# Kernel tuning notes

Hardware: AMD Instinct MI355X
Metric: run time of the kernel (lower is better)

The kernel has to match this reference:

```python
import jax, jax.numpy as jnp
import numpy as np

TOP_K = 4

def _silu_and_mul(gu):
    g, u = jnp.split(gu, 2, axis=-1)
    return jax.nn.silu(g) * u

def setup_inputs() -> dict:
    key = jax.random.key(0)
    ks = jax.random.split(key, 7)
    H, E, I, Is = 2048, 16, 1408, 5632
    s = 0.02
    return {
        "hidden_states": jax.random.normal(ks[0], (4, 1024, H), dtype=jnp.float32),
        "gate_w": jax.random.normal(ks[1], (E, H), dtype=jnp.float32) * s,
        "sgate_w": jax.random.normal(ks[2], (1, H), dtype=jnp.float32) * s,
        "w13": jax.random.normal(ks[3], (E, 2 * I, H), dtype=jnp.float32) * s,
        "w2": jax.random.normal(ks[4], (E, H, I), dtype=jnp.float32) * s,
        "shared_gate_up_w": jax.random.normal(ks[5], (2 * Is, H), dtype=jnp.float32) * s,
        "shared_down_w": jax.random.normal(ks[6], (H, Is), dtype=jnp.float32) * s,
    }

def reference(hidden_states, gate_w, sgate_w, w13, w2, shared_gate_up_w, shared_down_w):
    B, S, H = hidden_states.shape
    x = hidden_states.reshape(-1, H)  # [M, H]
    E = gate_w.shape[0]

    # shared expert: SiluAndMul MLP gated by sigmoid(shared_expert_gate(x))
    shared = _silu_and_mul(x @ shared_gate_up_w.T) @ shared_down_w.T
    shared = shared * jax.nn.sigmoid(x @ sgate_w.T)  # [M, H]

    # router: softmax in fp32, top-k (NOT renormalized, per original code)
    router_logits = x @ gate_w.T
    routing_weights = jax.nn.softmax(router_logits.astype(jnp.float32), axis=-1)
    topk_w, topk_ids = jax.lax.top_k(routing_weights, TOP_K)  # [M, K]

    # loop over fixed expert set via scan; every token goes through each
    # expert, masked by its routing coefficient (0 if not routed)
    def body(acc, ew):
        w13_e, w2_e, e = ew
        coef = jnp.sum(jnp.where(topk_ids == e, topk_w, 0.0), axis=-1)  # [M]
        h = _silu_and_mul(x @ w13_e.T)  # [M, I]
        acc = acc + (h @ w2_e.T).astype(jnp.float32) * coef[:, None]
        return acc, None

    init = jnp.zeros((x.shape[0], H), dtype=jnp.float32)
    sparse_out, _ = jax.lax.scan(body, init, (w13, w2, jnp.arange(E)))
    out = shared + sparse_out.astype(x.dtype)
    return out.reshape(B, S, H)
```

## Files before the change

kernel.cpp:

```cpp
#include <hip/hip_runtime.h>
#include <hip/hip_bf16.h>

#define E_NUM 16
#define TOPK 4
#define H_DIM 2048
#define I_DIM 1408
#define IS_DIM 5632
#define M_TOK 4096

typedef __attribute__((ext_vector_type(8))) short short8;
typedef __attribute__((ext_vector_type(4))) float f32x4;

static __device__ __forceinline__ unsigned short f2bf(float f) {
    unsigned int u = __float_as_uint(f);
    unsigned int r = (u + 0x7FFFu + ((u >> 16) & 1u)) >> 16;
    return (unsigned short)r;
}

static __device__ __forceinline__ void gl16(const unsigned short* g, unsigned short* l) {
    __builtin_amdgcn_global_load_lds(
        (const __attribute__((address_space(1))) unsigned int*)g,
        (__attribute__((address_space(3))) unsigned int*)l, 16, 0, 0);
}

__global__ __launch_bounds__(256) void k_router(
    const float* __restrict__ x, const float* __restrict__ gw,
    const float* __restrict__ sgw, int* __restrict__ counts,
    int* __restrict__ ltok, float* __restrict__ lcoef, float* __restrict__ sg)
{
    const int wid = threadIdx.x >> 6, lane = threadIdx.x & 63;
    const int t = blockIdx.x * 4 + wid;
    const float* xr = x + (size_t)t * H_DIM;
    float xv[32];
#pragma unroll
    for (int i = 0; i < 32; ++i) xv[i] = xr[i * 64 + lane];

    float lg[E_NUM];
    for (int e = 0; e < E_NUM; ++e) {
        const float* g = gw + (size_t)e * H_DIM;
        float s = 0.f;
#pragma unroll
        for (int i = 0; i < 32; ++i) s += xv[i] * g[i * 64 + lane];
#pragma unroll
        for (int off = 32; off; off >>= 1) s += __shfl_xor(s, off);
        lg[e] = s;
    }
    {
        float s = 0.f;
#pragma unroll
        for (int i = 0; i < 32; ++i) s += xv[i] * sgw[i * 64 + lane];
#pragma unroll
        for (int off = 32; off; off >>= 1) s += __shfl_xor(s, off);
        if (lane == 0) sg[t] = 1.f / (1.f + __expf(-s));
    }
    float mx = lg[0];
#pragma unroll
    for (int e = 1; e < E_NUM; ++e) mx = fmaxf(mx, lg[e]);
    float sum = 0.f, w[E_NUM];
#pragma unroll
    for (int e = 0; e < E_NUM; ++e) { w[e] = __expf(lg[e] - mx); sum += w[e]; }
    float inv = 1.f / sum;
#pragma unroll
    for (int e = 0; e < E_NUM; ++e) w[e] *= inv;

    if (lane == 0) {
        for (int j = 0; j < TOPK; ++j) {
            float best = -1.f; int bi = 0;
            for (int e = 0; e < E_NUM; ++e) if (w[e] > best) { best = w[e]; bi = e; }
            int pos = atomicAdd(&counts[bi], 1);
            ltok[bi * M_TOK + pos]  = t;
            lcoef[bi * M_TOK + pos] = best;
            w[bi] = -2.f;
        }
    }
}

__global__ void k_prefix(const int* __restrict__ counts, int* __restrict__ base) {
    if (threadIdx.x == 0) {
        int a = 0;
        for (int e = 0; e < E_NUM; ++e) { base[e] = a; a += counts[e]; }
        base[E_NUM] = a;
    }
}

__global__ __launch_bounds__(256) void k_cvtw(const float* __restrict__ src,
                                              unsigned short* __restrict__ dst, size_t n8)
{
    size_t stride = (size_t)gridDim.x * 256;
    for (size_t t = (size_t)blockIdx.x * 256 + threadIdx.x; t < n8; t += stride) {
        size_t i = t * 8;
        float4 a = *(const float4*)(src + i);
        float4 b = *(const float4*)(src + i + 4);
        union { unsigned short u[8]; short8 v; } o;
        o.u[0] = f2bf(a.x); o.u[1] = f2bf(a.y); o.u[2] = f2bf(a.z); o.u[3] = f2bf(a.w);
        o.u[4] = f2bf(b.x); o.u[5] = f2bf(b.y); o.u[6] = f2bf(b.z); o.u[7] = f2bf(b.w);
        *(short8*)(dst + i) = o.v;
    }
}

template<int MODE, int BN, int KDIM, int NOFF, long long BSTR, int KSPLIT>
__global__ __launch_bounds__(512, 2) void k_gemm(
    const unsigned short* __restrict__ Abase,
    const unsigned short* __restrict__ Bbase,
    void* __restrict__ outp,
    const int* __restrict__ ltok, const float* __restrict__ lcoef,
    const int* __restrict__ counts, const int* __restrict__ basearr,
    const float* __restrict__ sg)
{
    constexpr bool DUAL = (MODE == 0 || MODE == 2);
    constexpr int NFR = BN / 64;
    constexpr int KCH = KDIM / KSPLIT;

    extern __shared__ unsigned short smem[];
    unsigned short* sA = smem;
    unsigned short* sB = smem + 32768;

    const int tid = threadIdx.x;
    const int lane = tid & 63, wid = tid >> 6;
    const int wr = wid >> 2, wcol = wid & 3;
    const int lr = lane & 15, lk = lane >> 4;

    const unsigned gx = gridDim.x, gy = gridDim.y;
    const unsigned nwg = gx * gy;
    const unsigned orig = blockIdx.y * gx + blockIdx.x;
    const unsigned q8 = nwg >> 3, r8 = nwg & 7;
    const unsigned xcd = orig & 7, off8 = orig >> 3;
    const unsigned wg = ((xcd < r8) ? xcd * (q8 + 1) : r8 * (q8 + 1) + (xcd - r8) * q8) + off8;
    const int n0 = (int)(wg / gy) * BN;
    const int r0 = (int)(wg % gy) * 256;
    const int e  = blockIdx.z;

    int cnt = M_TOK, gbase = 0;
    if constexpr (MODE == 2 || MODE == 3) {
        cnt = counts[e];
        if (r0 >= cnt) return;
        gbase = basearr[e];
    }
    const int kbeg = (KSPLIT > 1) ? e * KCH : 0;
    const unsigned short* Bexp = Bbase + (size_t)e * (size_t)BSTR;

    const unsigned short* aptr[4];
    const unsigned short* bptr[4];
#pragma unroll
    for (int i = 0; i < 4; ++i) {
        const int c = i * 512 + tid;
        const int row = c >> 3, c8 = c & 7;
        int ar;
        if constexpr (MODE == 0 || MODE == 1) ar = r0 + row;
        else {
            int rr = r0 + row; if (rr > cnt - 1) rr = cnt - 1;
            ar = (MODE == 2) ? ltok[e * M_TOK + rr] : (gbase + rr);
        }
        aptr[i] = Abase + (size_t)ar * KDIM + kbeg + ((c8 ^ (row & 7)) << 3);
        int br;
        if constexpr (DUAL) br = (row < 128) ? (n0 + row) : (NOFF + n0 + row - 128);
        else br = n0 + row;
        bptr[i] = Bexp + (size_t)br * KDIM + kbeg + ((c8 ^ (row & 7)) << 3);
    }

    f32x4 acc[8][NFR];
    f32x4 accu[DUAL ? 8 : 1][NFR];
    const f32x4 z = {0.f, 0.f, 0.f, 0.f};
#pragma unroll
    for (int m = 0; m < 8; ++m)
#pragma unroll
        for (int n = 0; n < NFR; ++n) { acc[m][n] = z; if constexpr (DUAL) accu[m][n] = z; }

    auto STAGE = [&](int buf, int kt) {
        const int bo = buf << 14;
#pragma unroll
        for (int i = 0; i < 4; ++i) gl16(aptr[i] + kt, &sA[bo + ((i * 512 + tid) << 3)]);
#pragma unroll
        for (int i = 0; i < 4; ++i) gl16(bptr[i] + kt, &sB[bo + ((i * 512 + tid) << 3)]);
    };

    STAGE(0, 0);
    __syncthreads();
    int cur = 0;
#pragma unroll 1
    for (int kt = 0; kt < KCH; kt += 64) {
        if (kt + 64 < KCH) STAGE(cur ^ 1, kt + 64);
        __builtin_amdgcn_s_setprio(1);
#pragma unroll
        for (int kk = 0; kk < 2; ++kk) {
            const int c8 = kk * 4 + lk;
            short8 af[8];
#pragma unroll
            for (int m = 0; m < 8; ++m) {
                const int row = wr * 128 + m * 16 + lr;
                af[m] = *(const short8*)&sA[(cur << 14) + (row << 6) + ((c8 ^ (row & 7)) << 3)];
            }
#pragma unroll
            for (int n = 0; n < NFR; ++n) {
                const int rowb = wcol * (BN / 4) + n * 16 + lr;
                short8 bf = *(const short8*)&sB[(cur << 14) + (rowb << 6) + ((c8 ^ (rowb & 7)) << 3)];
#pragma unroll
                for (int m = 0; m < 8; ++m)
                    acc[m][n] = __builtin_amdgcn_mfma_f32_16x16x32_bf16(af[m], bf, acc[m][n], 0, 0, 0);
                if constexpr (DUAL) {
                    const int rowu = rowb + 128;
                    short8 bu = *(const short8*)&sB[(cur << 14) + (rowu << 6) + ((c8 ^ (rowu & 7)) << 3)];
#pragma unroll
                    for (int m = 0; m < 8; ++m)
                        accu[m][n] = __builtin_amdgcn_mfma_f32_16x16x32_bf16(af[m], bu, accu[m][n], 0, 0, 0);
                }
            }
        }
        __builtin_amdgcn_s_setprio(0);
        __syncthreads();
        cur ^= 1;
    }

    const int colbase = n0 + wcol * (BN / 4);
#pragma unroll
    for (int m = 0; m < 8; ++m) {
#pragma unroll
        for (int j = 0; j < 4; ++j) {
            const int r = wr * 128 + m * 16 + lk * 4 + j;
            if constexpr (MODE == 0) {
                size_t orow = (size_t)(r0 + r) * IS_DIM;
#pragma unroll
                for (int n = 0; n < NFR; ++n) {
                    int col = colbase + n * 16 + lr;
                    float g = acc[m][n][j];
                    float h = g / (1.f + __expf(-g)) * accu[m][n][j];
                    ((unsigned short*)outp)[orow + col] = f2bf(h);
                }
            } else if constexpr (MODE == 2) {
                if (r0 + r < cnt) {
                    size_t orow = (size_t)(gbase + r0 + r) * I_DIM;
#pragma unroll
                    for (int n = 0; n < NFR; ++n) {
                        int col = colbase + n * 16 + lr;
                        float g = acc[m][n][j];
                        float h = g / (1.f + __expf(-g)) * accu[m][n][j];
                        ((unsigned short*)outp)[orow + col] = f2bf(h);
                    }
                }
            } else if constexpr (MODE == 1) {
                int tok = r0 + r;
                float scale = sg[tok];
                size_t orow = (size_t)tok * H_DIM;
#pragma unroll
                for (int n = 0; n < NFR; ++n) {
                    int col = colbase + n * 16 + lr;
                    atomicAdd((float*)outp + orow + col, acc[m][n][j] * scale);
                }
            } else {
                if (r0 + r < cnt) {
                    int tok = ltok[e * M_TOK + r0 + r];
                    float scale = lcoef[e * M_TOK + r0 + r];
                    size_t orow = (size_t)tok * H_DIM;
#pragma unroll
                    for (int n = 0; n < NFR; ++n) {
                        int col = colbase + n * 16 + lr;
                        atomicAdd((float*)outp + orow + col, acc[m][n][j] * scale);
                    }
                }
            }
        }
    }
}

extern "C" void kernel_launch(void* const* d_in, const int* in_sizes, int n_in,
                              void* d_out, int out_size, void* d_ws, size_t ws_size,
                              hipStream_t stream) {
    const float* x    = (const float*)d_in[0];
    const float* gw   = (const float*)d_in[1];
    const float* sgw  = (const float*)d_in[2];
    const float* w13  = (const float*)d_in[3];
    const float* w2   = (const float*)d_in[4];
    const float* sguw = (const float*)d_in[5];
    const float* sdw  = (const float*)d_in[6];
    float* out = (float*)d_out;

    char* ws = (char*)d_ws;
    unsigned short* xb    = (unsigned short*)ws;
    unsigned short* hbuf  = (unsigned short*)(ws + 16777216);
    unsigned short* w13b  = (unsigned short*)(ws + 62914560);
    unsigned short* w2b   = (unsigned short*)(ws + 247463936);
    unsigned short* sguwb = (unsigned short*)(ws + 339738624);
    unsigned short* sdwb  = (unsigned short*)(ws + 385875968);
    size_t so = 408944640ULL;
    int*   ltok   = (int*)  (ws + so);
    float* lcoef  = (float*)(ws + so + 262144);
    int*   counts = (int*)  (ws + so + 524288);
    int*   basep  = (int*)  (ws + so + 524288 + 256);
    float* sg     = (float*)(ws + so + 524288 + 512);

    hipMemsetAsync(counts, 0, 64, stream);
    hipMemsetAsync(out, 0, (size_t)out_size * sizeof(float), stream);
    k_router<<<M_TOK / 4, 256, 0, stream>>>(x, gw, sgw, counts, ltok, lcoef, sg);
    k_prefix<<<1, 64, 0, stream>>>(counts, basep);
    k_cvtw<<<4096, 256, 0, stream>>>(x, xb, (size_t)M_TOK * H_DIM / 8);
    k_cvtw<<<8192, 256, 0, stream>>>(sguw, sguwb, (size_t)2 * IS_DIM * H_DIM / 8);
    k_cvtw<<<8192, 256, 0, stream>>>(sdw,  sdwb,  (size_t)H_DIM * IS_DIM / 8);
    k_cvtw<<<8192, 256, 0, stream>>>(w13,  w13b,  (size_t)E_NUM * 2 * I_DIM * H_DIM / 8);
    k_cvtw<<<8192, 256, 0, stream>>>(w2,   w2b,   (size_t)E_NUM * H_DIM * I_DIM / 8);

    static const int DYN = 131072;
    (void)hipFuncSetAttribute(reinterpret_cast<const void*>(&k_gemm<0, 128, 2048, IS_DIM, 0LL, 1>),
                              hipFuncAttributeMaxDynamicSharedMemorySize, DYN);
    (void)hipFuncSetAttribute(reinterpret_cast<const void*>(&k_gemm<1, 256, 5632, 0, 0LL, 2>),
                              hipFuncAttributeMaxDynamicSharedMemorySize, DYN);
    (void)hipFuncSetAttribute(reinterpret_cast<const void*>(&k_gemm<2, 128, 2048, I_DIM, 5767168LL, 1>),
                              hipFuncAttributeMaxDynamicSharedMemorySize, DYN);
    (void)hipFuncSetAttribute(reinterpret_cast<const void*>(&k_gemm<3, 256, 1408, 0, 2883584LL, 1>),
                              hipFuncAttributeMaxDynamicSharedMemorySize, DYN);

    k_gemm<0, 128, 2048, IS_DIM, 0LL, 1>
        <<<dim3(IS_DIM / 128, M_TOK / 256, 1), 512, DYN, stream>>>(
            xb, sguwb, hbuf, ltok, lcoef, counts, basep, sg);
    k_gemm<1, 256, 5632, 0, 0LL, 2>
        <<<dim3(H_DIM / 256, M_TOK / 256, 2), 512, DYN, stream>>>(
            hbuf, sdwb, out, ltok, lcoef, counts, basep, sg);
    k_gemm<2, 128, 2048, I_DIM, 5767168LL, 1>
        <<<dim3(I_DIM / 128, M_TOK / 256, E_NUM), 512, DYN, stream>>>(
            xb, w13b, hbuf, ltok, lcoef, counts, basep, sg);
    k_gemm<3, 256, 1408, 0, 2883584LL, 1>
        <<<dim3(H_DIM / 256, M_TOK / 256, E_NUM), 512, DYN, stream>>>(
            hbuf, w2b, out, ltok, lcoef, counts, basep, sg);
}
```

Baseline: 1.215 ms.

## Shrink GEMM tiles to 128x128 with 256 threads and single-buffered static LDS

Reworks the grouped GEMM kernel from 256-row tiles with 512 threads and double-buffered dynamic shared memory to 128x128 tiles with 256 threads and a single static LDS buffer. The intent is more workgroups and higher occupancy, which also wastes fewer padded rows for the variable per-expert token counts. In exchange it drops the prefetch overlap, so each K step now waits on its global loads before computing. Smaller tiles also mean less operand reuse per LDS load and more atomic traffic in the down projections.

```diff
diff --git a/kernel.cpp b/kernel.cpp
--- a/kernel.cpp
+++ b/kernel.cpp
@@ -98,8 +98,8 @@
     }
 }
 
-template<int MODE, int BN, int KDIM, int NOFF, long long BSTR, int KSPLIT>
-__global__ __launch_bounds__(512, 2) void k_gemm(
+template<int MODE, int KDIM, int NOFF, long long BSTR, int KSPLIT>
+__global__ __launch_bounds__(256, 2) void k_gemm(
     const unsigned short* __restrict__ Abase,
     const unsigned short* __restrict__ Bbase,
     void* __restrict__ outp,
@@ -108,16 +108,13 @@
     const float* __restrict__ sg)
 {
     constexpr bool DUAL = (MODE == 0 || MODE == 2);
-    constexpr int NFR = BN / 64;
+    constexpr int BROWS = DUAL ? 256 : 128;
+    constexpr int NB = BROWS / 32;
     constexpr int KCH = KDIM / KSPLIT;
-
-    extern __shared__ unsigned short smem[];
-    unsigned short* sA = smem;
-    unsigned short* sB = smem + 32768;
 
     const int tid = threadIdx.x;
     const int lane = tid & 63, wid = tid >> 6;
-    const int wr = wid >> 2, wcol = wid & 3;
+    const int wr = wid >> 1, wc = wid & 1;
     const int lr = lane & 15, lk = lane >> 4;
 
     const unsigned gx = gridDim.x, gy = gridDim.y;
@@ -126,8 +123,8 @@
     const unsigned q8 = nwg >> 3, r8 = nwg & 7;
     const unsigned xcd = orig & 7, off8 = orig >> 3;
     const unsigned wg = ((xcd < r8) ? xcd * (q8 + 1) : r8 * (q8 + 1) + (xcd - r8) * q8) + off8;
-    const int n0 = (int)(wg / gy) * BN;
-    const int r0 = (int)(wg % gy) * 256;
+    const int n0 = (int)(wg / gy) * 128;
+    const int r0 = (int)(wg % gy) * 128;
     const int e  = blockIdx.z;
 
     int cnt = M_TOK, gbase = 0;
@@ -139,11 +136,13 @@
     const int kbeg = (KSPLIT > 1) ? e * KCH : 0;
     const unsigned short* Bexp = Bbase + (size_t)e * (size_t)BSTR;
 
+    __shared__ unsigned short sA[128 * 64];
+    __shared__ unsigned short sB[BROWS * 64];
+
     const unsigned short* aptr[4];
-    const unsigned short* bptr[4];
 #pragma unroll
     for (int i = 0; i < 4; ++i) {
-        const int c = i * 512 + tid;
+        const int c = i * 256 + tid;
         const int row = c >> 3, c8 = c & 7;
         int ar;
         if constexpr (MODE == 0 || MODE == 1) ar = r0 + row;
@@ -152,75 +151,73 @@
             ar = (MODE == 2) ? ltok[e * M_TOK + rr] : (gbase + rr);
         }
         aptr[i] = Abase + (size_t)ar * KDIM + kbeg + ((c8 ^ (row & 7)) << 3);
+    }
+    const unsigned short* bptr[NB];
+#pragma unroll
+    for (int i = 0; i < NB; ++i) {
+        const int c = i * 256 + tid;
+        const int row = c >> 3, c8 = c & 7;
         int br;
         if constexpr (DUAL) br = (row < 128) ? (n0 + row) : (NOFF + n0 + row - 128);
         else br = n0 + row;
         bptr[i] = Bexp + (size_t)br * KDIM + kbeg + ((c8 ^ (row & 7)) << 3);
     }
 
-    f32x4 acc[8][NFR];
-    f32x4 accu[DUAL ? 8 : 1][NFR];
+    f32x4 acc[4][4];
+    f32x4 accu[DUAL ? 4 : 1][4];
     const f32x4 z = {0.f, 0.f, 0.f, 0.f};
 #pragma unroll
-    for (int m = 0; m < 8; ++m)
-#pragma unroll
-        for (int n = 0; n < NFR; ++n) { acc[m][n] = z; if constexpr (DUAL) accu[m][n] = z; }
-
-    auto STAGE = [&](int buf, int kt) {
-        const int bo = buf << 14;
-#pragma unroll
-        for (int i = 0; i < 4; ++i) gl16(aptr[i] + kt, &sA[bo + ((i * 512 + tid) << 3)]);
-#pragma unroll
-        for (int i = 0; i < 4; ++i) gl16(bptr[i] + kt, &sB[bo + ((i * 512 + tid) << 3)]);
-    };
-
-    STAGE(0, 0);
-    __syncthreads();
-    int cur = 0;
+    for (int m = 0; m < 4; ++m)
+#pragma unroll
+        for (int n = 0; n < 4; ++n) { acc[m][n] = z; if constexpr (DUAL) accu[m][n] = z; }
+
 #pragma unroll 1
     for (int kt = 0; kt < KCH; kt += 64) {
-        if (kt + 64 < KCH) STAGE(cur ^ 1, kt + 64);
+#pragma unroll
+        for (int i = 0; i < 4; ++i) gl16(aptr[i] + kt, &sA[(i * 256 + tid) << 3]);
+#pragma unroll
+        for (int i = 0; i < NB; ++i) gl16(bptr[i] + kt, &sB[(i * 256 + tid) << 3]);
+        __syncthreads();
         __builtin_amdgcn_s_setprio(1);
 #pragma unroll
         for (int kk = 0; kk < 2; ++kk) {
             const int c8 = kk * 4 + lk;
-            short8 af[8];
-#pragma unroll
-            for (int m = 0; m < 8; ++m) {
-                const int row = wr * 128 + m * 16 + lr;
-                af[m] = *(const short8*)&sA[(cur << 14) + (row << 6) + ((c8 ^ (row & 7)) << 3)];
+            short8 af[4];
+#pragma unroll
+            for (int m = 0; m < 4; ++m) {
+                const int row = wr * 64 + m * 16 + lr;
+                af[m] = *(const short8*)&sA[(row << 6) + ((c8 ^ (row & 7)) << 3)];
             }
 #pragma unroll
-            for (int n = 0; n < NFR; ++n) {
-                const int rowb = wcol * (BN / 4) + n * 16 + lr;
-                short8 bf = *(const short8*)&sB[(cur << 14) + (rowb << 6) + ((c8 ^ (rowb & 7)) << 3)];
-#pragma unroll
-                for (int m = 0; m < 8; ++m)
+            for (int n = 0; n < 4; ++n) {
+                const int rowb = wc * 64 + n * 16 + lr;
+                short8 bf = *(const short8*)&sB[(rowb << 6) + ((c8 ^ (rowb & 7)) << 3)];
+#pragma unroll
+                for (int m = 0; m < 4; ++m)
                     acc[m][n] = __builtin_amdgcn_mfma_f32_16x16x32_bf16(af[m], bf, acc[m][n], 0, 0, 0);
                 if constexpr (DUAL) {
                     const int rowu = rowb + 128;
-                    short8 bu = *(const short8*)&sB[(cur << 14) + (rowu << 6) + ((c8 ^ (rowu & 7)) << 3)];
-#pragma unroll
-                    for (int m = 0; m < 8; ++m)
+                    short8 bu = *(const short8*)&sB[(rowu << 6) + ((c8 ^ (rowu & 7)) << 3)];
+#pragma unroll
+                    for (int m = 0; m < 4; ++m)
                         accu[m][n] = __builtin_amdgcn_mfma_f32_16x16x32_bf16(af[m], bu, accu[m][n], 0, 0, 0);
                 }
             }
         }
         __builtin_amdgcn_s_setprio(0);
         __syncthreads();
-        cur ^= 1;
-    }
-
-    const int colbase = n0 + wcol * (BN / 4);
-#pragma unroll
-    for (int m = 0; m < 8; ++m) {
+    }
+
+    const int colbase = n0 + wc * 64;
+#pragma unroll
+    for (int m = 0; m < 4; ++m) {
 #pragma unroll
         for (int j = 0; j < 4; ++j) {
-            const int r = wr * 128 + m * 16 + lk * 4 + j;
+            const int r = wr * 64 + m * 16 + lk * 4 + j;
             if constexpr (MODE == 0) {
                 size_t orow = (size_t)(r0 + r) * IS_DIM;
 #pragma unroll
-                for (int n = 0; n < NFR; ++n) {
+                for (int n = 0; n < 4; ++n) {
                     int col = colbase + n * 16 + lr;
                     float g = acc[m][n][j];
                     float h = g / (1.f + __expf(-g)) * accu[m][n][j];
@@ -230,7 +227,7 @@
                 if (r0 + r < cnt) {
                     size_t orow = (size_t)(gbase + r0 + r) * I_DIM;
 #pragma unroll
-                    for (int n = 0; n < NFR; ++n) {
+                    for (int n = 0; n < 4; ++n) {
                         int col = colbase + n * 16 + lr;
                         float g = acc[m][n][j];
                         float h = g / (1.f + __expf(-g)) * accu[m][n][j];
@@ -242,7 +239,7 @@
                 float scale = sg[tok];
                 size_t orow = (size_t)tok * H_DIM;
 #pragma unroll
-                for (int n = 0; n < NFR; ++n) {
+                for (int n = 0; n < 4; ++n) {
                     int col = colbase + n * 16 + lr;
                     atomicAdd((float*)outp + orow + col, acc[m][n][j] * scale);
                 }
@@ -252,7 +249,7 @@
                     float scale = lcoef[e * M_TOK + r0 + r];
                     size_t orow = (size_t)tok * H_DIM;
 #pragma unroll
-                    for (int n = 0; n < NFR; ++n) {
+                    for (int n = 0; n < 4; ++n) {
                         int col = colbase + n * 16 + lr;
                         atomicAdd((float*)outp + orow + col, acc[m][n][j] * scale);
                     }
@@ -298,26 +295,16 @@
     k_cvtw<<<8192, 256, 0, stream>>>(w13,  w13b,  (size_t)E_NUM * 2 * I_DIM * H_DIM / 8);
     k_cvtw<<<8192, 256, 0, stream>>>(w2,   w2b,   (size_t)E_NUM * H_DIM * I_DIM / 8);
 
-    static const int DYN = 131072;
-    (void)hipFuncSetAttribute(reinterpret_cast<const void*>(&k_gemm<0, 128, 2048, IS_DIM, 0LL, 1>),
-                              hipFuncAttributeMaxDynamicSharedMemorySize, DYN);
-    (void)hipFuncSetAttribute(reinterpret_cast<const void*>(&k_gemm<1, 256, 5632, 0, 0LL, 2>),
-                              hipFuncAttributeMaxDynamicSharedMemorySize, DYN);
-    (void)hipFuncSetAttribute(reinterpret_cast<const void*>(&k_gemm<2, 128, 2048, I_DIM, 5767168LL, 1>),
-                              hipFuncAttributeMaxDynamicSharedMemorySize, DYN);
-    (void)hipFuncSetAttribute(reinterpret_cast<const void*>(&k_gemm<3, 256, 1408, 0, 2883584LL, 1>),
-                              hipFuncAttributeMaxDynamicSharedMemorySize, DYN);
-
-    k_gemm<0, 128, 2048, IS_DIM, 0LL, 1>
-        <<<dim3(IS_DIM / 128, M_TOK / 256, 1), 512, DYN, stream>>>(
+    k_gemm<0, 2048, IS_DIM, 0LL, 1>
+        <<<dim3(IS_DIM / 128, M_TOK / 128, 1), 256, 0, stream>>>(
             xb, sguwb, hbuf, ltok, lcoef, counts, basep, sg);
-    k_gemm<1, 256, 5632, 0, 0LL, 2>
-        <<<dim3(H_DIM / 256, M_TOK / 256, 2), 512, DYN, stream>>>(
+    k_gemm<1, 5632, 0, 0LL, 2>
+        <<<dim3(H_DIM / 128, M_TOK / 128, 2), 256, 0, stream>>>(
             hbuf, sdwb, out, ltok, lcoef, counts, basep, sg);
-    k_gemm<2, 128, 2048, I_DIM, 5767168LL, 1>
-        <<<dim3(I_DIM / 128, M_TOK / 256, E_NUM), 512, DYN, stream>>>(
+    k_gemm<2, 2048, I_DIM, 5767168LL, 1>
+        <<<dim3(I_DIM / 128, M_TOK / 128, E_NUM), 256, 0, stream>>>(
             xb, w13b, hbuf, ltok, lcoef, counts, basep, sg);
-    k_gemm<3, 256, 1408, 0, 2883584LL, 1>
-        <<<dim3(H_DIM / 256, M_TOK / 256, E_NUM), 512, DYN, stream>>>(
+    k_gemm<3, 1408, 0, 2883584LL, 1>
+        <<<dim3(H_DIM / 128, M_TOK / 128, E_NUM), 256, 0, stream>>>(
             hbuf, w2b, out, ltok, lcoef, counts, basep, sg);
 }
```

Result: no change. 1.230 ms (+1.2%).

## Interleave gate/up weight rows and pipeline GEMM in four quadrant sub-stages

Applied to the files above, without the earlier changes.

Adds a conversion kernel that reorders the gate/up weight rows into interleaved 16-row gate/up blocks, so the up-projection GEMMs can use a single uniform 256x256 tile instead of dual accumulators. The GEMM main loop is rebuilt into four quadrant phases, each issuing a half-tile prefetch for the next stage between LDS fragment loads and MFMA bursts, with explicit waitcnt and barrier at the end. The aim is to spread global-to-LDS traffic across the compute and lower accumulator register pressure. In exchange the kernel relies on the matching weight permutation, and its hand-written waitcnt/barrier ordering must be exactly right to avoid LDS races.

```diff
diff --git a/kernel.cpp b/kernel.cpp
--- a/kernel.cpp
+++ b/kernel.cpp
@@ -98,7 +98,30 @@
     }
 }
 
-template<int MODE, int BN, int KDIM, int NOFF, long long BSTR, int KSPLIT>
+template<int TWOI, int NOFF>
+__global__ __launch_bounds__(256) void k_cvtp(const float* __restrict__ src,
+                                              unsigned short* __restrict__ dst, size_t n8)
+{
+    size_t stride = (size_t)gridDim.x * 256;
+    for (size_t t = (size_t)blockIdx.x * 256 + threadIdx.x; t < n8; t += stride) {
+        size_t i = t * 8;
+        unsigned drow = (unsigned)(i >> 11);
+        unsigned col  = (unsigned)(i & 2047u);
+        unsigned grp = drow / (unsigned)TWOI;
+        unsigned rr  = drow - grp * (unsigned)TWOI;
+        unsigned q = rr >> 4, rm = rr & 15u;
+        unsigned srow = ((q >> 1) << 4) + rm + ((q & 1u) ? (unsigned)NOFF : 0u);
+        const float* s = src + (((size_t)grp * TWOI + srow) << 11) + col;
+        float4 a = *(const float4*)s;
+        float4 b = *(const float4*)(s + 4);
+        union { unsigned short u[8]; short8 v; } o;
+        o.u[0] = f2bf(a.x); o.u[1] = f2bf(a.y); o.u[2] = f2bf(a.z); o.u[3] = f2bf(a.w);
+        o.u[4] = f2bf(b.x); o.u[5] = f2bf(b.y); o.u[6] = f2bf(b.z); o.u[7] = f2bf(b.w);
+        *(short8*)(dst + i) = o.v;
+    }
+}
+
+template<int MODE, int KDIM, long long BSTR, int KSPLIT>
 __global__ __launch_bounds__(512, 2) void k_gemm(
     const unsigned short* __restrict__ Abase,
     const unsigned short* __restrict__ Bbase,
@@ -107,9 +130,10 @@
     const int* __restrict__ counts, const int* __restrict__ basearr,
     const float* __restrict__ sg)
 {
-    constexpr bool DUAL = (MODE == 0 || MODE == 2);
-    constexpr int NFR = BN / 64;
+    constexpr bool UP = (MODE == 0 || MODE == 2);
+    constexpr int OSTR = (MODE == 0) ? IS_DIM : I_DIM;
     constexpr int KCH = KDIM / KSPLIT;
+    constexpr int NT = KCH / 64;
 
     extern __shared__ unsigned short smem[];
     unsigned short* sA = smem;
@@ -126,7 +150,7 @@
     const unsigned q8 = nwg >> 3, r8 = nwg & 7;
     const unsigned xcd = orig & 7, off8 = orig >> 3;
     const unsigned wg = ((xcd < r8) ? xcd * (q8 + 1) : r8 * (q8 + 1) + (xcd - r8) * q8) + off8;
-    const int n0 = (int)(wg / gy) * BN;
+    const int n0 = (int)(wg / gy) * 256;
     const int r0 = (int)(wg % gy) * 256;
     const int e  = blockIdx.z;
 
@@ -139,122 +163,177 @@
     const int kbeg = (KSPLIT > 1) ? e * KCH : 0;
     const unsigned short* Bexp = Bbase + (size_t)e * (size_t)BSTR;
 
-    const unsigned short* aptr[4];
-    const unsigned short* bptr[4];
-#pragma unroll
-    for (int i = 0; i < 4; ++i) {
-        const int c = i * 512 + tid;
-        const int row = c >> 3, c8 = c & 7;
-        int ar;
-        if constexpr (MODE == 0 || MODE == 1) ar = r0 + row;
-        else {
-            int rr = r0 + row; if (rr > cnt - 1) rr = cnt - 1;
-            ar = (MODE == 2) ? ltok[e * M_TOK + rr] : (gbase + rr);
-        }
-        aptr[i] = Abase + (size_t)ar * KDIM + kbeg + ((c8 ^ (row & 7)) << 3);
-        int br;
-        if constexpr (DUAL) br = (row < 128) ? (n0 + row) : (NOFF + n0 + row - 128);
-        else br = n0 + row;
-        bptr[i] = Bexp + (size_t)br * KDIM + kbeg + ((c8 ^ (row & 7)) << 3);
-    }
-
-    f32x4 acc[8][NFR];
-    f32x4 accu[DUAL ? 8 : 1][NFR];
+    const unsigned short* aptr[2][2];
+    const unsigned short* bptr[2][2];
+#pragma unroll
+    for (int h = 0; h < 2; ++h) {
+#pragma unroll
+        for (int i = 0; i < 2; ++i) {
+            const int eo = (i * 512 + tid) * 8;
+            const int prow = eo >> 6;
+            const int kch = ((eo >> 3) & 7) ^ (prow & 7);
+            const int lrow = h * 128 + prow;
+            int ar;
+            if constexpr (MODE == 0 || MODE == 1) ar = r0 + lrow;
+            else {
+                int rr2 = r0 + lrow; if (rr2 > cnt - 1) rr2 = cnt - 1;
+                ar = (MODE == 2) ? ltok[e * M_TOK + rr2] : (gbase + rr2);
+            }
+            aptr[h][i] = Abase + (size_t)ar * KDIM + kbeg + kch * 8;
+            bptr[h][i] = Bexp + (size_t)(n0 + lrow) * KDIM + kbeg + kch * 8;
+        }
+    }
+
+    f32x4 acc[8][4];
     const f32x4 z = {0.f, 0.f, 0.f, 0.f};
 #pragma unroll
     for (int m = 0; m < 8; ++m)
 #pragma unroll
-        for (int n = 0; n < NFR; ++n) { acc[m][n] = z; if constexpr (DUAL) accu[m][n] = z; }
-
-    auto STAGE = [&](int buf, int kt) {
-        const int bo = buf << 14;
-#pragma unroll
-        for (int i = 0; i < 4; ++i) gl16(aptr[i] + kt, &sA[bo + ((i * 512 + tid) << 3)]);
-#pragma unroll
-        for (int i = 0; i < 4; ++i) gl16(bptr[i] + kt, &sB[bo + ((i * 512 + tid) << 3)]);
+        for (int n = 0; n < 4; ++n) acc[m][n] = z;
+
+    auto STAGEA = [&](int h, int buf, int kt) {
+#pragma unroll
+        for (int i = 0; i < 2; ++i)
+            gl16(aptr[h][i] + kt, &sA[buf * 16384 + h * 8192 + (i * 512 + tid) * 8]);
     };
-
-    STAGE(0, 0);
-    __syncthreads();
-    int cur = 0;
+    auto STAGEB = [&](int h, int buf, int kt) {
+#pragma unroll
+        for (int i = 0; i < 2; ++i)
+            gl16(bptr[h][i] + kt, &sB[buf * 16384 + h * 8192 + (i * 512 + tid) * 8]);
+    };
+
+    STAGEA(0, 0, 0); STAGEB(0, 0, 0); STAGEB(1, 0, 0); STAGEA(1, 0, 0);
+    asm volatile("s_waitcnt vmcnt(0)" ::: "memory");
+    __builtin_amdgcn_s_barrier();
+
+    short8 af[8], bfA[4], bfB[4];
+
 #pragma unroll 1
-    for (int kt = 0; kt < KCH; kt += 64) {
-        if (kt + 64 < KCH) STAGE(cur ^ 1, kt + 64);
+    for (int t = 0; t < NT; ++t) {
+        const int cur = t & 1, nxt = cur ^ 1;
+        const int kt1 = (t + 1) * 64;
+        const bool pf = (t + 1 < NT);
+        const int cb = cur * 16384;
+
+#pragma unroll
+        for (int m = 0; m < 4; ++m) {
+            const int row = wr * 64 + m * 16 + lr;
+#pragma unroll
+            for (int kk = 0; kk < 2; ++kk)
+                af[m * 2 + kk] = *(const short8*)&sA[cb + (row << 6) + ((((kk << 2) + lk) ^ (row & 7)) << 3)];
+        }
+#pragma unroll
+        for (int n = 0; n < 2; ++n) {
+            const int row = wcol * 32 + n * 16 + lr;
+#pragma unroll
+            for (int kk = 0; kk < 2; ++kk)
+                bfA[n * 2 + kk] = *(const short8*)&sB[cb + (row << 6) + ((((kk << 2) + lk) ^ (row & 7)) << 3)];
+        }
+        if (pf) STAGEA(0, nxt, kt1);
         __builtin_amdgcn_s_setprio(1);
 #pragma unroll
-        for (int kk = 0; kk < 2; ++kk) {
-            const int c8 = kk * 4 + lk;
-            short8 af[8];
-#pragma unroll
-            for (int m = 0; m < 8; ++m) {
-                const int row = wr * 128 + m * 16 + lr;
-                af[m] = *(const short8*)&sA[(cur << 14) + (row << 6) + ((c8 ^ (row & 7)) << 3)];
-            }
-#pragma unroll
-            for (int n = 0; n < NFR; ++n) {
-                const int rowb = wcol * (BN / 4) + n * 16 + lr;
-                short8 bf = *(const short8*)&sB[(cur << 14) + (rowb << 6) + ((c8 ^ (rowb & 7)) << 3)];
-#pragma unroll
-                for (int m = 0; m < 8; ++m)
-                    acc[m][n] = __builtin_amdgcn_mfma_f32_16x16x32_bf16(af[m], bf, acc[m][n], 0, 0, 0);
-                if constexpr (DUAL) {
-                    const int rowu = rowb + 128;
-                    short8 bu = *(const short8*)&sB[(cur << 14) + (rowu << 6) + ((c8 ^ (rowu & 7)) << 3)];
-#pragma unroll
-                    for (int m = 0; m < 8; ++m)
-                        accu[m][n] = __builtin_amdgcn_mfma_f32_16x16x32_bf16(af[m], bu, accu[m][n], 0, 0, 0);
+        for (int kk = 0; kk < 2; ++kk)
+#pragma unroll
+            for (int n = 0; n < 2; ++n)
+#pragma unroll
+                for (int m = 0; m < 4; ++m)
+                    acc[m][n] = __builtin_amdgcn_mfma_f32_16x16x32_bf16(af[m * 2 + kk], bfA[n * 2 + kk], acc[m][n], 0, 0, 0);
+        __builtin_amdgcn_s_setprio(0);
+
+#pragma unroll
+        for (int n = 0; n < 2; ++n) {
+            const int row = 128 + wcol * 32 + n * 16 + lr;
+#pragma unroll
+            for (int kk = 0; kk < 2; ++kk)
+                bfB[n * 2 + kk] = *(const short8*)&sB[cb + (row << 6) + ((((kk << 2) + lk) ^ (row & 7)) << 3)];
+        }
+        if (pf) STAGEB(0, nxt, kt1);
+        __builtin_amdgcn_s_setprio(1);
+#pragma unroll
+        for (int kk = 0; kk < 2; ++kk)
+#pragma unroll
+            for (int n = 0; n < 2; ++n)
+#pragma unroll
+                for (int m = 0; m < 4; ++m)
+                    acc[m][n + 2] = __builtin_amdgcn_mfma_f32_16x16x32_bf16(af[m * 2 + kk], bfB[n * 2 + kk], acc[m][n + 2], 0, 0, 0);
+        __builtin_amdgcn_s_setprio(0);
+
+#pragma unroll
+        for (int m = 0; m < 4; ++m) {
+            const int row = 128 + wr * 64 + m * 16 + lr;
+#pragma unroll
+            for (int kk = 0; kk < 2; ++kk)
+                af[m * 2 + kk] = *(const short8*)&sA[cb + (row << 6) + ((((kk << 2) + lk) ^ (row & 7)) << 3)];
+        }
+        if (pf) STAGEB(1, nxt, kt1);
+        __builtin_amdgcn_s_setprio(1);
+#pragma unroll
+        for (int kk = 0; kk < 2; ++kk)
+#pragma unroll
+            for (int n = 0; n < 2; ++n)
+#pragma unroll
+                for (int m = 0; m < 4; ++m)
+                    acc[m + 4][n] = __builtin_amdgcn_mfma_f32_16x16x32_bf16(af[m * 2 + kk], bfA[n * 2 + kk], acc[m + 4][n], 0, 0, 0);
+        __builtin_amdgcn_s_setprio(0);
+
+        if (pf) STAGEA(1, nxt, kt1);
+        __builtin_amdgcn_s_setprio(1);
+#pragma unroll
+        for (int kk = 0; kk < 2; ++kk)
+#pragma unroll
+            for (int n = 0; n < 2; ++n)
+#pragma unroll
+                for (int m = 0; m < 4; ++m)
+                    acc[m + 4][n + 2] = __builtin_amdgcn_mfma_f32_16x16x32_bf16(af[m * 2 + kk], bfB[n * 2 + kk], acc[m + 4][n + 2], 0, 0, 0);
+        __builtin_amdgcn_s_setprio(0);
+
+        asm volatile("s_waitcnt lgkmcnt(0)" ::: "memory");
+        asm volatile("s_waitcnt vmcnt(0)" ::: "memory");
+        __builtin_amdgcn_s_barrier();
+    }
+
+    if constexpr (UP) {
+        const int hc0 = (n0 >> 1) + wcol * 16 + lr;
+        unsigned short* hb = (unsigned short*)outp;
+#pragma unroll
+        for (int m = 0; m < 8; ++m) {
+            const int rb = (m < 4 ? wr * 64 + m * 16 : 128 + wr * 64 + (m - 4) * 16) + lk * 4;
+#pragma unroll
+            for (int j = 0; j < 4; ++j) {
+                const int r = rb + j;
+                bool ok; size_t orow;
+                if constexpr (MODE == 0) { ok = true; orow = (size_t)(r0 + r) * OSTR; }
+                else { ok = (r0 + r < cnt); orow = (size_t)(gbase + r0 + r) * OSTR; }
+                if (ok) {
+                    float g0 = acc[m][0][j], u0 = acc[m][1][j];
+                    float g1 = acc[m][2][j], u1 = acc[m][3][j];
+                    hb[orow + hc0]      = f2bf(g0 / (1.f + __expf(-g0)) * u0);
+                    hb[orow + hc0 + 64] = f2bf(g1 / (1.f + __expf(-g1)) * u1);
                 }
             }
         }
-        __builtin_amdgcn_s_setprio(0);
-        __syncthreads();
-        cur ^= 1;
-    }
-
-    const int colbase = n0 + wcol * (BN / 4);
-#pragma unroll
-    for (int m = 0; m < 8; ++m) {
-#pragma unroll
-        for (int j = 0; j < 4; ++j) {
-            const int r = wr * 128 + m * 16 + lk * 4 + j;
-            if constexpr (MODE == 0) {
-                size_t orow = (size_t)(r0 + r) * IS_DIM;
-#pragma unroll
-                for (int n = 0; n < NFR; ++n) {
-                    int col = colbase + n * 16 + lr;
-                    float g = acc[m][n][j];
-                    float h = g / (1.f + __expf(-g)) * accu[m][n][j];
-                    ((unsigned short*)outp)[orow + col] = f2bf(h);
+    } else {
+        float* op = (float*)outp;
+#pragma unroll
+        for (int m = 0; m < 8; ++m) {
+            const int rb = (m < 4 ? wr * 64 + m * 16 : 128 + wr * 64 + (m - 4) * 16) + lk * 4;
+#pragma unroll
+            for (int j = 0; j < 4; ++j) {
+                const int r = rb + j;
+                int tok; float scale; bool ok;
+                if constexpr (MODE == 1) {
+                    tok = r0 + r; scale = sg[tok]; ok = true;
+                } else {
+                    ok = (r0 + r < cnt);
+                    int idx = ok ? (e * M_TOK + r0 + r) : (e * M_TOK);
+                    tok = ltok[idx]; scale = lcoef[idx];
                 }
-            } else if constexpr (MODE == 2) {
-                if (r0 + r < cnt) {
-                    size_t orow = (size_t)(gbase + r0 + r) * I_DIM;
-#pragma unroll
-                    for (int n = 0; n < NFR; ++n) {
-                        int col = colbase + n * 16 + lr;
-                        float g = acc[m][n][j];
-                        float h = g / (1.f + __expf(-g)) * accu[m][n][j];
-                        ((unsigned short*)outp)[orow + col] = f2bf(h);
-                    }
-                }
-            } else if constexpr (MODE == 1) {
-                int tok = r0 + r;
-                float scale = sg[tok];
-                size_t orow = (size_t)tok * H_DIM;
-#pragma unroll
-                for (int n = 0; n < NFR; ++n) {
-                    int col = colbase + n * 16 + lr;
-                    atomicAdd((float*)outp + orow + col, acc[m][n][j] * scale);
-                }
-            } else {
-                if (r0 + r < cnt) {
-                    int tok = ltok[e * M_TOK + r0 + r];
-                    float scale = lcoef[e * M_TOK + r0 + r];
+                if (ok) {
                     size_t orow = (size_t)tok * H_DIM;
 #pragma unroll
-                    for (int n = 0; n < NFR; ++n) {
-                        int col = colbase + n * 16 + lr;
-                        atomicAdd((float*)outp + orow + col, acc[m][n][j] * scale);
+                    for (int n = 0; n < 4; ++n) {
+                        const int col = n0 + (n < 2 ? wcol * 32 + n * 16 : 128 + wcol * 32 + (n - 2) * 16) + lr;
+                        atomicAdd(op + orow + col, acc[m][n][j] * scale);
                     }
                 }
             }
@@ -293,31 +372,31 @@
     k_router<<<M_TOK / 4, 256, 0, stream>>>(x, gw, sgw, counts, ltok, lcoef, sg);
     k_prefix<<<1, 64, 0, stream>>>(counts, basep);
     k_cvtw<<<4096, 256, 0, stream>>>(x, xb, (size_t)M_TOK * H_DIM / 8);
-    k_cvtw<<<8192, 256, 0, stream>>>(sguw, sguwb, (size_t)2 * IS_DIM * H_DIM / 8);
+    k_cvtp<2 * IS_DIM, IS_DIM><<<8192, 256, 0, stream>>>(sguw, sguwb, (size_t)2 * IS_DIM * H_DIM / 8);
     k_cvtw<<<8192, 256, 0, stream>>>(sdw,  sdwb,  (size_t)H_DIM * IS_DIM / 8);
-    k_cvtw<<<8192, 256, 0, stream>>>(w13,  w13b,  (size_t)E_NUM * 2 * I_DIM * H_DIM / 8);
+    k_cvtp<2 * I_DIM, I_DIM><<<8192, 256, 0, stream>>>(w13, w13b, (size_t)E_NUM * 2 * I_DIM * H_DIM / 8);
     k_cvtw<<<8192, 256, 0, stream>>>(w2,   w2b,   (size_t)E_NUM * H_DIM * I_DIM / 8);
 
     static const int DYN = 131072;
-    (void)hipFuncSetAttribute(reinterpret_cast<const void*>(&k_gemm<0, 128, 2048, IS_DIM, 0LL, 1>),
+    (void)hipFuncSetAttribute(reinterpret_cast<const void*>(&k_gemm<0, 2048, 0LL, 1>),
                               hipFuncAttributeMaxDynamicSharedMemorySize, DYN);
-    (void)hipFuncSetAttribute(reinterpret_cast<const void*>(&k_gemm<1, 256, 5632, 0, 0LL, 2>),
+    (void)hipFuncSetAttribute(reinterpret_cast<const void*>(&k_gemm<1, 5632, 0LL, 2>),
                               hipFuncAttributeMaxDynamicSharedMemorySize, DYN);
-    (void)hipFuncSetAttribute(reinterpret_cast<const void*>(&k_gemm<2, 128, 2048, I_DIM, 5767168LL, 1>),
+    (void)hipFuncSetAttribute(reinterpret_cast<const void*>(&k_gemm<2, 2048, 5767168LL, 1>),
                               hipFuncAttributeMaxDynamicSharedMemorySize, DYN);
-    (void)hipFuncSetAttribute(reinterpret_cast<const void*>(&k_gemm<3, 256, 1408, 0, 2883584LL, 1>),
+    (void)hipFuncSetAttribute(reinterpret_cast<const void*>(&k_gemm<3, 1408, 2883584LL, 1>),
                               hipFuncAttributeMaxDynamicSharedMemorySize, DYN);
 
-    k_gemm<0, 128, 2048, IS_DIM, 0LL, 1>
-        <<<dim3(IS_DIM / 128, M_TOK / 256, 1), 512, DYN, stream>>>(
+    k_gemm<0, 2048, 0LL, 1>
+        <<<dim3(2 * IS_DIM / 256, M_TOK / 256, 1), 512, DYN, stream>>>(
             xb, sguwb, hbuf, ltok, lcoef, counts, basep, sg);
-    k_gemm<1, 256, 5632, 0, 0LL, 2>
+    k_gemm<1, 5632, 0LL, 2>
         <<<dim3(H_DIM / 256, M_TOK / 256, 2), 512, DYN, stream>>>(
             hbuf, sdwb, out, ltok, lcoef, counts, basep, sg);
-    k_gemm<2, 128, 2048, I_DIM, 5767168LL, 1>
-        <<<dim3(I_DIM / 128, M_TOK / 256, E_NUM), 512, DYN, stream>>>(
+    k_gemm<2, 2048, 5767168LL, 1>
+        <<<dim3(2 * I_DIM / 256, M_TOK / 256, E_NUM), 512, DYN, stream>>>(
             xb, w13b, hbuf, ltok, lcoef, counts, basep, sg);
-    k_gemm<3, 256, 1408, 0, 2883584LL, 1>
+    k_gemm<3, 1408, 2883584LL, 1>
         <<<dim3(H_DIM / 256, M_TOK / 256, E_NUM), 512, DYN, stream>>>(
             hbuf, w2b, out, ltok, lcoef, counts, basep, sg);
 }
```

Measured after the change: 1.278 ms. +5.1%, slower.
